# Kernel optimization log

Hardware: AMD Instinct MI355X
Metric: run time of the kernel (lower is better)

## Reference

```python
import jax, jax.numpy as jnp
import numpy as np

B, S, D, R, H, NI, NP, NO, K = 2, 2048, 1024, 1024, 8, 8, 32, 8, 3
DH = R // H


def setup_inputs() -> dict:
    key = jax.random.key(0)
    ks = jax.random.split(key, 32)
    rn = lambda k, shp, s=1.0: jax.random.normal(k, shp, jnp.float32) * s
    nrm = lambda v: v / (jnp.linalg.norm(v, axis=-1, keepdims=True) + 1e-8)
    w = 1.0 / np.sqrt(D).astype(np.float32)
    inp = {
        'x': rn(ks[0], (B, S, D)),
        'mask': jnp.tril(jnp.ones((S, S), bool))[None, None],  # causal [1,1,S,S]
        'Wr_in': rn(ks[1], (NI, D), w), 'Wr_proc': rn(ks[2], (NP, D), w), 'Wr_out': rn(ks[3], (NO, D), w),
        'WrO_in': rn(ks[4], (NI, R), w), 'WrO_proc': rn(ks[5], (NP, R), w), 'WrO_out': rn(ks[6], (NO, R), w),
        'Wq_in': rn(ks[7], (NI, D, R), w), 'vq': nrm(rn(ks[8], (NP, R))), 'Wq_out': rn(ks[9], (NO, R, D), w),
        'Wk_in': rn(ks[10], (NI, D, R), w), 'vk': nrm(rn(ks[11], (NP, R))), 'Wk_out': rn(ks[12], (NO, R, D), w),
        'Wv_in': rn(ks[13], (NI, D, R), w), 'vv': nrm(rn(ks[14], (NP, R))), 'Wv_out': rn(ks[15], (NO, R, D), w),
        # circuit_O = NeuronCircuit(rank, d_model): dims swapped
        'Wo_in': rn(ks[16], (NI, R, D), w), 'vo': nrm(rn(ks[17], (NP, D))), 'Wo_out': rn(ks[18], (NO, D, R), w),
    }
    return inp


def _router(x, Wi, Wp, Wo, k):
    in_w = jax.nn.softmax(x @ Wi.T, axis=-1)            # [B,S,NI]
    _, proc_idx = jax.lax.top_k(x @ Wp.T, k)            # [B,S,k]
    out_w = jax.nn.softmax(x @ Wo.T, axis=-1)           # [B,S,NO]
    return in_w, proc_idx, out_w


def _circuit(x, Win, vproc, Wout, in_w, proc_idx, out_w):
    # soft input mix: d_in -> r
    h = jnp.einsum('bsd,ndr,bsn->bsr', x, Win, in_w)
    # k sequential Householder reflections with gathered vectors
    v = vproc[proc_idx]                                 # [B,S,k,r]
    v = v / jnp.sqrt(jnp.sum(v * v, axis=-1, keepdims=True) + 1e-8)
    for i in range(v.shape[2]):
        vi = v[:, :, i, :]
        h = h - 2.0 * vi * jnp.sum(h * vi, axis=-1, keepdims=True)
    # soft output mix: r -> d_out
    return jnp.einsum('bsr,nrd,bsn->bsd', h, Wout, out_w)


def reference(x, mask, Wr_in, Wr_proc, Wr_out, WrO_in, WrO_proc, WrO_out,
              Wq_in, vq, Wq_out, Wk_in, vk, Wk_out, Wv_in, vv, Wv_out,
              Wo_in, vo, Wo_out):
    in_w, pidx, out_w = _router(x, Wr_in, Wr_proc, Wr_out, K)
    Q = _circuit(x, Wq_in, vq, Wq_out, in_w, pidx, out_w)   # [B,S,R]
    Kt = _circuit(x, Wk_in, vk, Wk_out, in_w, pidx, out_w)
    V = _circuit(x, Wv_in, vv, Wv_out, in_w, pidx, out_w)
    q = Q.reshape(B, S, H, DH).transpose(0, 2, 1, 3)
    k = Kt.reshape(B, S, H, DH).transpose(0, 2, 1, 3)
    v = V.reshape(B, S, H, DH).transpose(0, 2, 1, 3)
    scores = jnp.einsum('bhqd,bhkd->bhqk', q, k) / np.sqrt(DH).astype(np.float32)
    scores = jnp.where(mask, scores, jnp.float32(-1e9))
    p = jax.nn.softmax(scores, axis=-1)
    o = jnp.einsum('bhqk,bhkd->bhqd', p, v)
    o = o.transpose(0, 2, 1, 3).reshape(B, S, R)
    in_wO, pidxO, out_wO = _router(o, WrO_in, WrO_proc, WrO_out, K)
    out = _circuit(o, Wo_in, vo, Wo_out, in_wO, pidxO, out_wO)  # [B,S,D]
    return out
```

## Files before the change

### kernel.cpp

```cpp
#include <hip/hip_runtime.h>


typedef __attribute__((ext_vector_type(4))) float f32x4;
typedef _Float16 f16x8 __attribute__((ext_vector_type(8)));
typedef _Float16 f16x4 __attribute__((ext_vector_type(4)));

static constexpr int S_LEN  = 2048;
static constexpr int TOK    = 4096;
static constexpr int DMODEL = 1024;
static constexpr int KDIM   = 8192;

__device__ __forceinline__ void async16(const void* g, void* l) {
  __builtin_amdgcn_global_load_lds(
      (const __attribute__((address_space(1))) void*)g,
      (__attribute__((address_space(3))) void*)l, 16, 0, 0);
}

__global__ __launch_bounds__(256) void split_kernel(const float* __restrict__ X,
                                                    _Float16* __restrict__ Xh,
                                                    _Float16* __restrict__ Xl) {
  size_t i = ((size_t)blockIdx.x * 256 + threadIdx.x) * 4;
  float4 v = *(const float4*)&X[i];
  float a[4] = {v.x, v.y, v.z, v.w};
  f16x4 hv, lv;
#pragma unroll
  for (int e = 0; e < 4; ++e) {
    _Float16 hh = (_Float16)a[e];
    hv[e] = hh;
    lv[e] = (_Float16)(a[e] - (float)hh);
  }
  *(f16x4*)&Xh[i] = hv;
  *(f16x4*)&Xl[i] = lv;
}

__global__ __launch_bounds__(256) void transpose_split(const float* __restrict__ W,
                                                       _Float16* __restrict__ Th,
                                                       _Float16* __restrict__ Tl) {
  __shared__ float tbuf[64][65];
  const int tid = threadIdx.x;
  const int k0 = blockIdx.x * 64, n0 = blockIdx.y * 64;
#pragma unroll
  for (int j = 0; j < 4; ++j) {
    int ci = tid + 256 * j;
    int r = ci >> 4, c4 = (ci & 15) * 4;
    float4 v = *(const float4*)&W[(size_t)(k0 + r) * DMODEL + n0 + c4];
    tbuf[r][c4 + 0] = v.x; tbuf[r][c4 + 1] = v.y;
    tbuf[r][c4 + 2] = v.z; tbuf[r][c4 + 3] = v.w;
  }
  __syncthreads();
#pragma unroll
  for (int j = 0; j < 2; ++j) {
    int ci = tid + 256 * j;
    int nl = ci >> 3, k8 = (ci & 7) * 8;
    f16x8 hv, lv;
#pragma unroll
    for (int e = 0; e < 8; ++e) {
      float v = tbuf[k8 + e][nl];
      _Float16 hh = (_Float16)v;
      hv[e] = hh;
      lv[e] = (_Float16)(v - (float)hh);
    }
    size_t off = (size_t)(n0 + nl) * KDIM + k0 + k8;
    *(f16x8*)&Th[off] = hv;
    *(f16x8*)&Tl[off] = lv;
  }
}

__global__ __launch_bounds__(256) void router_kernel(const float* __restrict__ X,
                                                     const float* __restrict__ Wi,
                                                     const float* __restrict__ Wp,
                                                     const float* __restrict__ Wo,
                                                     float* __restrict__ in_w,
                                                     float* __restrict__ out_w,
                                                     int* __restrict__ pidx) {
  __shared__ float xs[1024];
  __shared__ double lg[48];
  const int t = blockIdx.x, tid = threadIdx.x;
  const int wid = tid >> 6, lane = tid & 63;
#pragma unroll
  for (int j = 0; j < 4; ++j) {
    int d = tid + 256 * j;
    xs[d] = X[(size_t)t * DMODEL + d];
  }
  __syncthreads();
  for (int i = wid; i < 48; i += 4) {
    const float* wrow = (i < 8)  ? Wi + (size_t)i * DMODEL
                      : (i < 40) ? Wp + (size_t)(i - 8) * DMODEL
                                 : Wo + (size_t)(i - 40) * DMODEL;
    double s = 0.0;
#pragma unroll
    for (int j = 0; j < 16; ++j) { int d = lane + 64 * j; s += (double)xs[d] * (double)wrow[d]; }
#pragma unroll
    for (int mm = 32; mm >= 1; mm >>= 1) s += __shfl_xor(s, mm);
    if (lane == 0) lg[i] = s;
  }
  __syncthreads();
  if (tid == 0) {
    float l[8], m;
    for (int i = 0; i < 8; ++i) l[i] = (float)lg[i];
    m = l[0];
    for (int i = 1; i < 8; ++i) m = fmaxf(m, l[i]);
    float e[8], su = 0.f;
    for (int i = 0; i < 8; ++i) { e[i] = expf(l[i] - m); su += e[i]; }
    for (int i = 0; i < 8; ++i) in_w[t * 8 + i] = e[i] / su;
  } else if (tid == 64) {
    float l[8], m;
    for (int i = 0; i < 8; ++i) l[i] = (float)lg[40 + i];
    m = l[0];
    for (int i = 1; i < 8; ++i) m = fmaxf(m, l[i]);
    float e[8], su = 0.f;
    for (int i = 0; i < 8; ++i) { e[i] = expf(l[i] - m); su += e[i]; }
    for (int i = 0; i < 8; ++i) out_w[t * 8 + i] = e[i] / su;
  } else if (tid == 128) {
    unsigned used = 0;
    for (int j = 0; j < 3; ++j) {
      double best = -1e300; int bi = 0;
      for (int i = 0; i < 32; ++i)
        if (!((used >> i) & 1u) && lg[8 + i] > best) { best = lg[8 + i]; bi = i; }
      used |= 1u << bi;
      pidx[t * 3 + j] = bi;
    }
  }
}

__global__ __launch_bounds__(256) void reflect_kernel(const float* __restrict__ Pa,
                                                      const float* __restrict__ Pb,
                                                      const int* __restrict__ pidx,
                                                      const float* __restrict__ vtab,
                                                      _Float16* __restrict__ Hh,
                                                      _Float16* __restrict__ Hl) {
  __shared__ float red[8];
  const int t = blockIdx.x, tid = threadIdx.x;
  const int wid = tid >> 6, lane = tid & 63;
  float4 ha = *(const float4*)&Pa[(size_t)t * DMODEL + tid * 4];
  float4 hb = *(const float4*)&Pb[(size_t)t * DMODEL + tid * 4];
  float4 h = {ha.x + hb.x, ha.y + hb.y, ha.z + hb.z, ha.w + hb.w};
  for (int i = 0; i < 3; ++i) {
    int idx = pidx[t * 3 + i];
    float4 vi = *(const float4*)&vtab[(size_t)idx * DMODEL + tid * 4];
    float hv = h.x * vi.x + h.y * vi.y + h.z * vi.z + h.w * vi.w;
    float vv = vi.x * vi.x + vi.y * vi.y + vi.z * vi.z + vi.w * vi.w;
#pragma unroll
    for (int mm = 32; mm >= 1; mm >>= 1) { hv += __shfl_xor(hv, mm); vv += __shfl_xor(vv, mm); }
    if (lane == 0) { red[wid] = hv; red[4 + wid] = vv; }
    __syncthreads();
    float dot = red[0] + red[1] + red[2] + red[3];
    float vn  = red[4] + red[5] + red[6] + red[7];
    __syncthreads();
    float c = 2.f * dot / (vn + 1e-8f);
    h.x -= c * vi.x; h.y -= c * vi.y; h.z -= c * vi.z; h.w -= c * vi.w;
  }
  float a[4] = {h.x, h.y, h.z, h.w};
  f16x4 hv4, lv4;
#pragma unroll
  for (int e = 0; e < 4; ++e) {
    _Float16 hh = (_Float16)a[e];
    hv4[e] = hh;
    lv4[e] = (_Float16)(a[e] - (float)hh);
  }
  *(f16x4*)&Hh[(size_t)t * DMODEL + tid * 4] = hv4;
  *(f16x4*)&Hl[(size_t)t * DMODEL + tid * 4] = lv4;
}

__global__ __launch_bounds__(256) void reduce_add(const float* __restrict__ a,
                                                  const float* __restrict__ b,
                                                  float* __restrict__ c) {
  size_t i = ((size_t)blockIdx.x * 256 + threadIdx.x) * 4;
  float4 va = *(const float4*)&a[i];
  float4 vb = *(const float4*)&b[i];
  float4 vc = {va.x + vb.x, va.y + vb.y, va.z + vb.z, va.w + vb.w};
  *(float4*)&c[i] = vc;
}

__global__ __launch_bounds__(256, 4) void gemm_planes(const _Float16* __restrict__ Ahp,
                                                      const _Float16* __restrict__ Alp,
                                                      const float* __restrict__ wmix,
                                                      const _Float16* __restrict__ Bh,
                                                      const _Float16* __restrict__ Bl,
                                                      float* __restrict__ Cp0,
                                                      float* __restrict__ Cp1) {
  __shared__ _Float16 sAh[128 * 32], sAl[128 * 32];
  __shared__ _Float16 sBh[128 * 32], sBl[128 * 32];
  __shared__ float sWr[128 * 4];
  const int tid = threadIdx.x;
  const int wid = tid >> 6, lane = tid & 63;
  const int l16 = lane & 15, lhi = lane >> 4;
  const int wr = wid >> 1, wc = wid & 1;
  const int fid = blockIdx.x + (blockIdx.y << 5) + (blockIdx.z << 8);
  const int wg  = ((fid & 7) << 6) + (fid >> 3);
  const int bm = (wg & 31) * 128;
  const int bn = ((wg >> 5) & 7) * 128;
  const int kz = wg >> 8;
  const int kbase = kz * 4096, nb = kz * 4;
  float* __restrict__ Cp = kz ? Cp1 : Cp0;

  for (int i = tid; i < 512; i += 256) {
    int row = i >> 2, p = i & 3;
    const float* w = &wmix[(size_t)(bm + row) * 8 + nb];
    sWr[i] = (p < 3) ? w[p] / w[p + 1] : w[3];
  }

  f32x4 acc[4][4];
#pragma unroll
  for (int i = 0; i < 4; ++i)
#pragma unroll
    for (int j = 0; j < 4; ++j) { f32x4 z = {0.f, 0.f, 0.f, 0.f}; acc[i][j] = z; }

  for (int kt = 0; kt < 4096; kt += 32) {
    const int kg = kbase + kt, d0 = kg & 1023;
#pragma unroll
    for (int j = 0; j < 2; ++j) {
      int ci = tid + 256 * j;
      int row = ci >> 2, jc = ci & 3;
      int jcs = jc ^ ((row >> 1) & 3);
      size_t ga = (size_t)(bm + row) * DMODEL + d0 + jcs * 8;
      size_t gb = (size_t)(bn + row) * KDIM + kg + jcs * 8;
      async16(&Ahp[ga], &sAh[ci * 8]);
      async16(&Alp[ga], &sAl[ci * 8]);
      async16(&Bh[gb], &sBh[ci * 8]);
      async16(&Bl[gb], &sBl[ci * 8]);
    }
    __syncthreads();
    f16x8 fah[4], fal[4], fbh[4], fbl[4];
#pragma unroll
    for (int mi = 0; mi < 4; ++mi) {
      int row = wr * 64 + mi * 16 + l16;
      int idx = row * 32 + ((lhi ^ ((row >> 1) & 3)) * 8);
      fah[mi] = *(const f16x8*)&sAh[idx];
      fal[mi] = *(const f16x8*)&sAl[idx];
    }
#pragma unroll
    for (int ni = 0; ni < 4; ++ni) {
      int row = wc * 64 + ni * 16 + l16;
      int idx = row * 32 + ((lhi ^ ((row >> 1) & 3)) * 8);
      fbh[ni] = *(const f16x8*)&sBh[idx];
      fbl[ni] = *(const f16x8*)&sBl[idx];
    }
#pragma unroll
    for (int mi = 0; mi < 4; ++mi)
#pragma unroll
      for (int ni = 0; ni < 4; ++ni) {
        f32x4 a = acc[mi][ni];
        a = __builtin_amdgcn_mfma_f32_16x16x32_f16(fah[mi], fbh[ni], a, 0, 0, 0);
        a = __builtin_amdgcn_mfma_f32_16x16x32_f16(fah[mi], fbl[ni], a, 0, 0, 0);
        a = __builtin_amdgcn_mfma_f32_16x16x32_f16(fal[mi], fbh[ni], a, 0, 0, 0);
        acc[mi][ni] = a;
      }
    __syncthreads();
    if ((kt & 1023) == 992 && kt != 4064) {
      int p = kt >> 10;
#pragma unroll
      for (int mi = 0; mi < 4; ++mi)
#pragma unroll
        for (int r = 0; r < 4; ++r) {
          float s = sWr[(wr * 64 + mi * 16 + lhi * 4 + r) * 4 + p];
#pragma unroll
          for (int ni = 0; ni < 4; ++ni) acc[mi][ni][r] *= s;
        }
    }
  }
#pragma unroll
  for (int mi = 0; mi < 4; ++mi)
#pragma unroll
    for (int r = 0; r < 4; ++r) {
      int rowl = wr * 64 + mi * 16 + lhi * 4 + r;
      float s = sWr[rowl * 4 + 3];
#pragma unroll
      for (int ni = 0; ni < 4; ++ni) {
        int col = bn + wc * 64 + ni * 16 + l16;
        Cp[(size_t)(bm + rowl) * DMODEL + col] = acc[mi][ni][r] * s;
      }
    }
}

__global__ __launch_bounds__(256) void vtrans_kernel(const float* __restrict__ Va,
                                                     const float* __restrict__ Vb,
                                                     float* __restrict__ Vt) {
  __shared__ float tbuf[64][65];
  const int tid = threadIdx.x;
  const int t0 = blockIdx.x * 64, d0 = blockIdx.y * 64, bh = blockIdx.z;
  const int b = bh >> 3, h = bh & 7;
#pragma unroll
  for (int j = 0; j < 4; ++j) {
    int ci = tid + 256 * j;
    int r = ci >> 4, c4 = (ci & 15) * 4;
    size_t g = (size_t)(b * S_LEN + t0 + r) * DMODEL + h * 128 + d0 + c4;
    float4 va = *(const float4*)&Va[g];
    float4 vb = *(const float4*)&Vb[g];
    tbuf[r][c4 + 0] = va.x + vb.x; tbuf[r][c4 + 1] = va.y + vb.y;
    tbuf[r][c4 + 2] = va.z + vb.z; tbuf[r][c4 + 3] = va.w + vb.w;
  }
  __syncthreads();
#pragma unroll
  for (int j = 0; j < 4; ++j) {
    int ci = tid + 256 * j;
    int r = ci >> 4, c4 = (ci & 15) * 4;
    float4 o;
    o.x = tbuf[c4 + 0][r]; o.y = tbuf[c4 + 1][r];
    o.z = tbuf[c4 + 2][r]; o.w = tbuf[c4 + 3][r];
    *(float4*)&Vt[((size_t)bh * 128 + d0 + r) * S_LEN + t0 + c4] = o;
  }
}

__global__ __launch_bounds__(256) void attn_kernel(const float* __restrict__ Q,
                                                   const float* __restrict__ Kg,
                                                   const float* __restrict__ Vt,
                                                   float* __restrict__ O,
                                                   _Float16* __restrict__ Oh,
                                                   _Float16* __restrict__ Ol) {
  __shared__ _Float16 sKh[32 * 128], sKl[32 * 128];
  __shared__ _Float16 sVh[128 * 32], sVl[128 * 32];
  __shared__ _Float16 sPh[4 * 16 * 32], sPl[4 * 16 * 32];
  const int tid = threadIdx.x;
  const int wid = tid >> 6, lane = tid & 63;
  const int l16 = lane & 15, lhi = lane >> 4;
  const int qt = (gridDim.x - 1) - blockIdx.x;
  const int bh = blockIdx.y;
  const int b = bh >> 3, h = bh & 7;
  const size_t qkbase = (size_t)b * S_LEN * DMODEL + h * 128;
  const float scale = 0.08838834764831845f;

  const int qrow = qt * 64 + wid * 16 + l16;
  f16x8 qh[4], ql[4];
#pragma unroll
  for (int kk = 0; kk < 4; ++kk) {
    const float* qp = &Q[qkbase + (size_t)qrow * DMODEL + kk * 32 + lhi * 8];
    float4 a = *(const float4*)qp;
    float4 c = *(const float4*)(qp + 4);
    float v[8] = {a.x, a.y, a.z, a.w, c.x, c.y, c.z, c.w};
#pragma unroll
    for (int e = 0; e < 8; ++e) {
      _Float16 hh = (_Float16)v[e];
      qh[kk][e] = hh;
      ql[kk][e] = (_Float16)(v[e] - (float)hh);
    }
  }

  f32x4 of[8];
#pragma unroll
  for (int i = 0; i < 8; ++i) { f32x4 z = {0.f, 0.f, 0.f, 0.f}; of[i] = z; }
  float m_[4], l_[4];
#pragma unroll
  for (int r = 0; r < 4; ++r) { m_[r] = -1e30f; l_[r] = 0.f; }

  const int ntw = qt * 2 + 1 + (wid >> 1);
  const int NT  = qt * 2 + 2;

  for (int kt = 0; kt < NT; ++kt) {
    __syncthreads();
#pragma unroll
    for (int j = 0; j < 4; ++j) {
      int ci = tid + 256 * j;
      int k = ci >> 5, d4 = (ci & 31) * 4;
      float4 v = *(const float4*)&Kg[qkbase + (size_t)(kt * 32 + k) * DMODEL + d4];
      f16x4 hv, lv;
      float vals[4] = {v.x, v.y, v.z, v.w};
#pragma unroll
      for (int e = 0; e < 4; ++e) {
        _Float16 hh = (_Float16)vals[e];
        hv[e] = hh;
        lv[e] = (_Float16)(vals[e] - (float)hh);
      }
      int idx = k * 128 + (d4 ^ ((k & 7) * 8));
      *(f16x4*)&sKh[idx] = hv;
      *(f16x4*)&sKl[idx] = lv;
    }
#pragma unroll
    for (int j = 0; j < 4; ++j) {
      int ci = tid + 256 * j;
      int d = ci >> 3, t4 = (ci & 7) * 4;
      float4 v = *(const float4*)&Vt[((size_t)bh * 128 + d) * S_LEN + kt * 32 + t4];
      f16x4 hv, lv;
      float vals[4] = {v.x, v.y, v.z, v.w};
#pragma unroll
      for (int e = 0; e < 4; ++e) {
        _Float16 hh = (_Float16)vals[e];
        hv[e] = hh;
        lv[e] = (_Float16)(vals[e] - (float)hh);
      }
      int idx = d * 32 + (t4 ^ (((d >> 1) & 3) * 8));
      *(f16x4*)&sVh[idx] = hv;
      *(f16x4*)&sVl[idx] = lv;
    }
    __syncthreads();

    if (kt < ntw) {
      f32x4 s0 = {0.f, 0.f, 0.f, 0.f}, s1 = {0.f, 0.f, 0.f, 0.f};
#pragma unroll
      for (int kk = 0; kk < 4; ++kk) {
        int col = (kk * 32 + lhi * 8);
        int i0 = l16 * 128 + (col ^ ((l16 & 7) * 8));
        int i1 = (16 + l16) * 128 + (col ^ (((16 + l16) & 7) * 8));
        f16x8 kb0h = *(const f16x8*)&sKh[i0];
        f16x8 kb0l = *(const f16x8*)&sKl[i0];
        f16x8 kb1h = *(const f16x8*)&sKh[i1];
        f16x8 kb1l = *(const f16x8*)&sKl[i1];
        s0 = __builtin_amdgcn_mfma_f32_16x16x32_f16(qh[kk], kb0h, s0, 0, 0, 0);
        s0 = __builtin_amdgcn_mfma_f32_16x16x32_f16(qh[kk], kb0l, s0, 0, 0, 0);
        s0 = __builtin_amdgcn_mfma_f32_16x16x32_f16(ql[kk], kb0h, s0, 0, 0, 0);
        s1 = __builtin_amdgcn_mfma_f32_16x16x32_f16(qh[kk], kb1h, s1, 0, 0, 0);
        s1 = __builtin_amdgcn_mfma_f32_16x16x32_f16(qh[kk], kb1l, s1, 0, 0, 0);
        s1 = __builtin_amdgcn_mfma_f32_16x16x32_f16(ql[kk], kb1h, s1, 0, 0, 0);
      }
      const int qg = qt * 64 + wid * 16 + (lane >> 4) * 4;
      if (kt == ntw - 1) {
#pragma unroll
        for (int r = 0; r < 4; ++r) {
          int q = qg + r;
          int k0 = kt * 32 + l16, k1 = k0 + 16;
          s0[r] = (k0 <= q) ? s0[r] * scale : -1e30f;
          s1[r] = (k1 <= q) ? s1[r] * scale : -1e30f;
        }
      } else {
#pragma unroll
        for (int r = 0; r < 4; ++r) { s0[r] *= scale; s1[r] *= scale; }
      }
      float p0[4], p1[4], fr[4];
#pragma unroll
      for (int r = 0; r < 4; ++r) {
        float rm = fmaxf(s0[r], s1[r]);
        rm = fmaxf(rm, __shfl_xor(rm, 1));
        rm = fmaxf(rm, __shfl_xor(rm, 2));
        rm = fmaxf(rm, __shfl_xor(rm, 4));
        rm = fmaxf(rm, __shfl_xor(rm, 8));
        float mn = fmaxf(m_[r], rm);
        fr[r] = __expf(m_[r] - mn);
        m_[r] = mn;
        p0[r] = __expf(s0[r] - mn);
        p1[r] = __expf(s1[r] - mn);
        float rs = p0[r] + p1[r];
        rs += __shfl_xor(rs, 1);
        rs += __shfl_xor(rs, 2);
        rs += __shfl_xor(rs, 4);
        rs += __shfl_xor(rs, 8);
        l_[r] = l_[r] * fr[r] + rs;
      }
#pragma unroll
      for (int i = 0; i < 8; ++i)
#pragma unroll
        for (int r = 0; r < 4; ++r) of[i][r] *= fr[r];
#pragma unroll
      for (int r = 0; r < 4; ++r) {
        int q = (lane >> 4) * 4 + r;
        int swz = ((q >> 1) & 3) * 8;
        int c0 = l16, c1 = 16 + l16;
        _Float16 h0 = (_Float16)p0[r];
        _Float16 h1 = (_Float16)p1[r];
        sPh[wid * 512 + q * 32 + (c0 ^ swz)] = h0;
        sPl[wid * 512 + q * 32 + (c0 ^ swz)] = (_Float16)(p0[r] - (float)h0);
        sPh[wid * 512 + q * 32 + (c1 ^ swz)] = h1;
        sPl[wid * 512 + q * 32 + (c1 ^ swz)] = (_Float16)(p1[r] - (float)h1);
      }
      int pidxr = wid * 512 + l16 * 32 + ((lhi * 8) ^ (((l16 >> 1) & 3) * 8));
      f16x8 pah = *(const f16x8*)&sPh[pidxr];
      f16x8 pal = *(const f16x8*)&sPl[pidxr];
#pragma unroll
      for (int d16 = 0; d16 < 8; ++d16) {
        int d = d16 * 16 + l16;
        int vidx = d * 32 + ((lhi * 8) ^ (((d >> 1) & 3) * 8));
        f16x8 vbh = *(const f16x8*)&sVh[vidx];
        f16x8 vbl = *(const f16x8*)&sVl[vidx];
        f32x4 a = of[d16];
        a = __builtin_amdgcn_mfma_f32_16x16x32_f16(pah, vbh, a, 0, 0, 0);
        a = __builtin_amdgcn_mfma_f32_16x16x32_f16(pah, vbl, a, 0, 0, 0);
        a = __builtin_amdgcn_mfma_f32_16x16x32_f16(pal, vbh, a, 0, 0, 0);
        of[d16] = a;
      }
    }
  }
  float inv[4];
#pragma unroll
  for (int r = 0; r < 4; ++r) inv[r] = 1.f / l_[r];
  const int qg = qt * 64 + wid * 16 + (lane >> 4) * 4;
#pragma unroll
  for (int d16 = 0; d16 < 8; ++d16)
#pragma unroll
    for (int r = 0; r < 4; ++r) {
      float val = of[d16][r] * inv[r];
      size_t gi = qkbase + (size_t)(qg + r) * DMODEL + d16 * 16 + l16;
      O[gi] = val;
      _Float16 hh = (_Float16)val;
      Oh[gi] = hh;
      Ol[gi] = (_Float16)(val - (float)hh);
    }
}

extern "C" void kernel_launch(void* const* d_in, const int* in_sizes, int n_in,
                              void* d_out, int out_size, void* d_ws, size_t ws_size,
                              hipStream_t stream) {
  (void)in_sizes; (void)n_in; (void)out_size;
  const float* x        = (const float*)d_in[0];
  const float* Wr_in    = (const float*)d_in[2];
  const float* Wr_proc  = (const float*)d_in[3];
  const float* Wr_out   = (const float*)d_in[4];
  const float* WrO_in   = (const float*)d_in[5];
  const float* WrO_proc = (const float*)d_in[6];
  const float* WrO_out  = (const float*)d_in[7];
  const float* Wq_in    = (const float*)d_in[8];
  const float* vq       = (const float*)d_in[9];
  const float* Wq_out   = (const float*)d_in[10];
  const float* Wk_in    = (const float*)d_in[11];
  const float* vk       = (const float*)d_in[12];
  const float* Wk_out   = (const float*)d_in[13];
  const float* Wv_in    = (const float*)d_in[14];
  const float* vv       = (const float*)d_in[15];
  const float* Wv_out   = (const float*)d_in[16];
  const float* Wo_in    = (const float*)d_in[17];
  const float* vo       = (const float*)d_in[18];
  const float* Wo_out   = (const float*)d_in[19];

  char* wsbase = (char*)d_ws;
  size_t off = 0;
  auto carve = [&](size_t bytes) -> void* {
    void* r = wsbase + off;
    off = (off + bytes + 255) & ~(size_t)255;
    return r;
  };
  const size_t WBYTES = (size_t)KDIM * DMODEL * 2;
  const size_t PBYTES = (size_t)TOK * DMODEL * 2;
  const size_t HBYTES = (size_t)TOK * DMODEL * 4;
  _Float16* WTh = (_Float16*)carve(WBYTES);
  _Float16* WTl = (_Float16*)carve(WBYTES);
  _Float16* Xh  = (_Float16*)carve(PBYTES);
  _Float16* Xl  = (_Float16*)carve(PBYTES);
  _Float16* Hh  = (_Float16*)carve(PBYTES);
  _Float16* Hl  = (_Float16*)carve(PBYTES);
  float* c0 = (float*)carve(HBYTES);
  float* c1 = (float*)carve(HBYTES);
  float* r1 = (float*)carve(HBYTES);
  float* r2 = (float*)carve(HBYTES);
  float* iw1 = (float*)carve((size_t)TOK * 8 * 4);
  float* ow1 = (float*)carve((size_t)TOK * 8 * 4);
  float* iw2 = (float*)carve((size_t)TOK * 8 * 4);
  float* ow2 = (float*)carve((size_t)TOK * 8 * 4);
  int* pi1 = (int*)carve((size_t)TOK * 3 * 4);
  int* pi2 = (int*)carve((size_t)TOK * 3 * 4);

  if (off > ws_size) {
    hipMemsetAsync(d_out, 0, (size_t)out_size * 4, stream);
    return;
  }

  float* Vt = (float*)WTh;
  _Float16* Oh = (_Float16*)r1;
  _Float16* Ol = Oh + (size_t)TOK * DMODEL;

  const dim3 blk(256);
  const dim3 tgrid(KDIM / 64, DMODEL / 64);
  const dim3 ggrid(TOK / 128, DMODEL / 128, 2);
  const dim3 rgrid(TOK * DMODEL / (256 * 4));
  const dim3 vgrid(S_LEN / 64, 2, 16);
  const dim3 agrid(S_LEN / 64, 16);

  split_kernel<<<rgrid, blk, 0, stream>>>(x, Xh, Xl);
  router_kernel<<<TOK, blk, 0, stream>>>(x, Wr_in, Wr_proc, Wr_out, iw1, ow1, pi1);

  transpose_split<<<tgrid, blk, 0, stream>>>(Wq_in, WTh, WTl);
  gemm_planes<<<ggrid, blk, 0, stream>>>(Xh, Xl, iw1, WTh, WTl, c0, c1);
  reflect_kernel<<<TOK, blk, 0, stream>>>(c0, c1, pi1, vq, Hh, Hl);
  transpose_split<<<tgrid, blk, 0, stream>>>(Wq_out, WTh, WTl);
  gemm_planes<<<ggrid, blk, 0, stream>>>(Hh, Hl, ow1, WTh, WTl, c0, c1);
  reduce_add<<<rgrid, blk, 0, stream>>>(c0, c1, r1);

  transpose_split<<<tgrid, blk, 0, stream>>>(Wk_in, WTh, WTl);
  gemm_planes<<<ggrid, blk, 0, stream>>>(Xh, Xl, iw1, WTh, WTl, c0, c1);
  reflect_kernel<<<TOK, blk, 0, stream>>>(c0, c1, pi1, vk, Hh, Hl);
  transpose_split<<<tgrid, blk, 0, stream>>>(Wk_out, WTh, WTl);
  gemm_planes<<<ggrid, blk, 0, stream>>>(Hh, Hl, ow1, WTh, WTl, c0, c1);
  reduce_add<<<rgrid, blk, 0, stream>>>(c0, c1, r2);

  transpose_split<<<tgrid, blk, 0, stream>>>(Wv_in, WTh, WTl);
  gemm_planes<<<ggrid, blk, 0, stream>>>(Xh, Xl, iw1, WTh, WTl, c0, c1);
  reflect_kernel<<<TOK, blk, 0, stream>>>(c0, c1, pi1, vv, Hh, Hl);
  transpose_split<<<tgrid, blk, 0, stream>>>(Wv_out, WTh, WTl);
  gemm_planes<<<ggrid, blk, 0, stream>>>(Hh, Hl, ow1, WTh, WTl, c0, c1);
  vtrans_kernel<<<vgrid, blk, 0, stream>>>(c0, c1, Vt);

  attn_kernel<<<agrid, blk, 0, stream>>>(r1, r2, Vt, c0, Oh, Ol);

  router_kernel<<<TOK, blk, 0, stream>>>(c0, WrO_in, WrO_proc, WrO_out, iw2, ow2, pi2);
  transpose_split<<<tgrid, blk, 0, stream>>>(Wo_in, WTh, WTl);
  gemm_planes<<<ggrid, blk, 0, stream>>>(Oh, Ol, iw2, WTh, WTl, c1, r2);
  reflect_kernel<<<TOK, blk, 0, stream>>>(c1, r2, pi2, vo, Hh, Hl);
  transpose_split<<<tgrid, blk, 0, stream>>>(Wo_out, WTh, WTl);
  gemm_planes<<<ggrid, blk, 0, stream>>>(Hh, Hl, ow2, WTh, WTl, c0, c1);
  reduce_add<<<rgrid, blk, 0, stream>>>(c0, c1, (float*)d_out);
}
```

Baseline: 1.934 ms.

## Split GEMM K into three chunks, prequantize Q/K/V planes, drop low-A MFMA in output circuit

The split-K GEMM now uses three K partitions (3072/3072/2048) instead of two. This grows the grid from 512 to 768 workgroups to fill more CUs, and the reflect/reduce kernels now sum three partials. Q, K and V are converted to fp16 hi/lo planes once in the reduce and transpose kernels, so attention loads them with async global-to-LDS copies instead of converting on every tile. The final circuit's GEMMs use a FAST variant that skips the low-A plane and its MFMA, and attention writes only the fp16-hi O. This trades some accuracy in the last stage for less MFMA work and memory traffic.

```diff
diff --git a/kernel.cpp b/kernel.cpp
--- a/kernel.cpp
+++ b/kernel.cpp
@@ -123,18 +123,22 @@
   }
 }
 
-__global__ __launch_bounds__(256) void reflect_kernel(const float* __restrict__ Pa,
-                                                      const float* __restrict__ Pb,
-                                                      const int* __restrict__ pidx,
-                                                      const float* __restrict__ vtab,
-                                                      _Float16* __restrict__ Hh,
-                                                      _Float16* __restrict__ Hl) {
+__global__ __launch_bounds__(256) void reflect3_kernel(const float* __restrict__ Pa,
+                                                       const float* __restrict__ Pb,
+                                                       const float* __restrict__ Pc,
+                                                       const int* __restrict__ pidx,
+                                                       const float* __restrict__ vtab,
+                                                       _Float16* __restrict__ Hh,
+                                                       _Float16* __restrict__ Hl) {
   __shared__ float red[8];
   const int t = blockIdx.x, tid = threadIdx.x;
   const int wid = tid >> 6, lane = tid & 63;
-  float4 ha = *(const float4*)&Pa[(size_t)t * DMODEL + tid * 4];
-  float4 hb = *(const float4*)&Pb[(size_t)t * DMODEL + tid * 4];
-  float4 h = {ha.x + hb.x, ha.y + hb.y, ha.z + hb.z, ha.w + hb.w};
+  size_t gi = (size_t)t * DMODEL + tid * 4;
+  float4 ha = *(const float4*)&Pa[gi];
+  float4 hb = *(const float4*)&Pb[gi];
+  float4 hc = *(const float4*)&Pc[gi];
+  float4 h = {ha.x + hb.x + hc.x, ha.y + hb.y + hc.y,
+              ha.z + hb.z + hc.z, ha.w + hb.w + hc.w};
   for (int i = 0; i < 3; ++i) {
     int idx = pidx[t * 3 + i];
     float4 vi = *(const float4*)&vtab[(size_t)idx * DMODEL + tid * 4];
@@ -158,27 +162,54 @@
     hv4[e] = hh;
     lv4[e] = (_Float16)(a[e] - (float)hh);
   }
-  *(f16x4*)&Hh[(size_t)t * DMODEL + tid * 4] = hv4;
-  *(f16x4*)&Hl[(size_t)t * DMODEL + tid * 4] = lv4;
-}
-
-__global__ __launch_bounds__(256) void reduce_add(const float* __restrict__ a,
-                                                  const float* __restrict__ b,
-                                                  float* __restrict__ c) {
+  *(f16x4*)&Hh[gi] = hv4;
+  *(f16x4*)&Hl[gi] = lv4;
+}
+
+__global__ __launch_bounds__(256) void reduce3_planes(const float* __restrict__ a,
+                                                      const float* __restrict__ b,
+                                                      const float* __restrict__ c,
+                                                      _Float16* __restrict__ Dh,
+                                                      _Float16* __restrict__ Dl) {
   size_t i = ((size_t)blockIdx.x * 256 + threadIdx.x) * 4;
   float4 va = *(const float4*)&a[i];
   float4 vb = *(const float4*)&b[i];
-  float4 vc = {va.x + vb.x, va.y + vb.y, va.z + vb.z, va.w + vb.w};
-  *(float4*)&c[i] = vc;
-}
-
+  float4 vc = *(const float4*)&c[i];
+  float s[4] = {va.x + vb.x + vc.x, va.y + vb.y + vc.y,
+                va.z + vb.z + vc.z, va.w + vb.w + vc.w};
+  f16x4 hv, lv;
+#pragma unroll
+  for (int e = 0; e < 4; ++e) {
+    _Float16 hh = (_Float16)s[e];
+    hv[e] = hh;
+    lv[e] = (_Float16)(s[e] - (float)hh);
+  }
+  *(f16x4*)&Dh[i] = hv;
+  *(f16x4*)&Dl[i] = lv;
+}
+
+__global__ __launch_bounds__(256) void reduce3_f32(const float* __restrict__ a,
+                                                   const float* __restrict__ b,
+                                                   const float* __restrict__ c,
+                                                   float* __restrict__ d) {
+  size_t i = ((size_t)blockIdx.x * 256 + threadIdx.x) * 4;
+  float4 va = *(const float4*)&a[i];
+  float4 vb = *(const float4*)&b[i];
+  float4 vc = *(const float4*)&c[i];
+  float4 vd = {va.x + vb.x + vc.x, va.y + vb.y + vc.y,
+               va.z + vb.z + vc.z, va.w + vb.w + vc.w};
+  *(float4*)&d[i] = vd;
+}
+
+template <bool FAST>
 __global__ __launch_bounds__(256, 4) void gemm_planes(const _Float16* __restrict__ Ahp,
                                                       const _Float16* __restrict__ Alp,
                                                       const float* __restrict__ wmix,
                                                       const _Float16* __restrict__ Bh,
                                                       const _Float16* __restrict__ Bl,
-                                                      float* __restrict__ Cp0,
-                                                      float* __restrict__ Cp1) {
+                                                      float* __restrict__ C0,
+                                                      float* __restrict__ C1,
+                                                      float* __restrict__ C2) {
   __shared__ _Float16 sAh[128 * 32], sAl[128 * 32];
   __shared__ _Float16 sBh[128 * 32], sBl[128 * 32];
   __shared__ float sWr[128 * 4];
@@ -187,17 +218,19 @@
   const int l16 = lane & 15, lhi = lane >> 4;
   const int wr = wid >> 1, wc = wid & 1;
   const int fid = blockIdx.x + (blockIdx.y << 5) + (blockIdx.z << 8);
-  const int wg  = ((fid & 7) << 6) + (fid >> 3);
-  const int bm = (wg & 31) * 128;
-  const int bn = ((wg >> 5) & 7) * 128;
-  const int kz = wg >> 8;
-  const int kbase = kz * 4096, nb = kz * 4;
-  float* __restrict__ Cp = kz ? Cp1 : Cp0;
+  const int wg  = (fid & 7) * 96 + (fid >> 3);
+  const int kz  = wg >> 8;
+  const int rem = wg & 255;
+  const int bm = (rem & 31) * 128;
+  const int bn = (rem >> 5) * 128;
+  const int np = (kz == 2) ? 2 : 3;
+  const int kbase = kz * 3072, nb = kz * 3;
+  float* __restrict__ Cp = (kz == 0) ? C0 : (kz == 1) ? C1 : C2;
 
   for (int i = tid; i < 512; i += 256) {
     int row = i >> 2, p = i & 3;
     const float* w = &wmix[(size_t)(bm + row) * 8 + nb];
-    sWr[i] = (p < 3) ? w[p] / w[p + 1] : w[3];
+    sWr[i] = (p < np - 1) ? w[p] / w[p + 1] : w[np - 1];
   }
 
   f32x4 acc[4][4];
@@ -206,7 +239,8 @@
 #pragma unroll
     for (int j = 0; j < 4; ++j) { f32x4 z = {0.f, 0.f, 0.f, 0.f}; acc[i][j] = z; }
 
-  for (int kt = 0; kt < 4096; kt += 32) {
+  const int kend = np * 1024;
+  for (int kt = 0; kt < kend; kt += 32) {
     const int kg = kbase + kt, d0 = kg & 1023;
 #pragma unroll
     for (int j = 0; j < 2; ++j) {
@@ -216,7 +250,7 @@
       size_t ga = (size_t)(bm + row) * DMODEL + d0 + jcs * 8;
       size_t gb = (size_t)(bn + row) * KDIM + kg + jcs * 8;
       async16(&Ahp[ga], &sAh[ci * 8]);
-      async16(&Alp[ga], &sAl[ci * 8]);
+      if (!FAST) async16(&Alp[ga], &sAl[ci * 8]);
       async16(&Bh[gb], &sBh[ci * 8]);
       async16(&Bl[gb], &sBl[ci * 8]);
     }
@@ -227,7 +261,7 @@
       int row = wr * 64 + mi * 16 + l16;
       int idx = row * 32 + ((lhi ^ ((row >> 1) & 3)) * 8);
       fah[mi] = *(const f16x8*)&sAh[idx];
-      fal[mi] = *(const f16x8*)&sAl[idx];
+      if (!FAST) fal[mi] = *(const f16x8*)&sAl[idx];
     }
 #pragma unroll
     for (int ni = 0; ni < 4; ++ni) {
@@ -243,11 +277,12 @@
         f32x4 a = acc[mi][ni];
         a = __builtin_amdgcn_mfma_f32_16x16x32_f16(fah[mi], fbh[ni], a, 0, 0, 0);
         a = __builtin_amdgcn_mfma_f32_16x16x32_f16(fah[mi], fbl[ni], a, 0, 0, 0);
-        a = __builtin_amdgcn_mfma_f32_16x16x32_f16(fal[mi], fbh[ni], a, 0, 0, 0);
+        if (!FAST)
+          a = __builtin_amdgcn_mfma_f32_16x16x32_f16(fal[mi], fbh[ni], a, 0, 0, 0);
         acc[mi][ni] = a;
       }
     __syncthreads();
-    if ((kt & 1023) == 992 && kt != 4064) {
+    if ((kt & 1023) == 992 && kt != kend - 32) {
       int p = kt >> 10;
 #pragma unroll
       for (int mi = 0; mi < 4; ++mi)
@@ -273,9 +308,11 @@
     }
 }
 
-__global__ __launch_bounds__(256) void vtrans_kernel(const float* __restrict__ Va,
-                                                     const float* __restrict__ Vb,
-                                                     float* __restrict__ Vt) {
+__global__ __launch_bounds__(256) void vtrans3_kernel(const float* __restrict__ Va,
+                                                      const float* __restrict__ Vb,
+                                                      const float* __restrict__ Vc,
+                                                      _Float16* __restrict__ Vth,
+                                                      _Float16* __restrict__ Vtl) {
   __shared__ float tbuf[64][65];
   const int tid = threadIdx.x;
   const int t0 = blockIdx.x * 64, d0 = blockIdx.y * 64, bh = blockIdx.z;
@@ -287,27 +324,37 @@
     size_t g = (size_t)(b * S_LEN + t0 + r) * DMODEL + h * 128 + d0 + c4;
     float4 va = *(const float4*)&Va[g];
     float4 vb = *(const float4*)&Vb[g];
-    tbuf[r][c4 + 0] = va.x + vb.x; tbuf[r][c4 + 1] = va.y + vb.y;
-    tbuf[r][c4 + 2] = va.z + vb.z; tbuf[r][c4 + 3] = va.w + vb.w;
+    float4 vc = *(const float4*)&Vc[g];
+    tbuf[r][c4 + 0] = va.x + vb.x + vc.x; tbuf[r][c4 + 1] = va.y + vb.y + vc.y;
+    tbuf[r][c4 + 2] = va.z + vb.z + vc.z; tbuf[r][c4 + 3] = va.w + vb.w + vc.w;
   }
   __syncthreads();
 #pragma unroll
   for (int j = 0; j < 4; ++j) {
     int ci = tid + 256 * j;
     int r = ci >> 4, c4 = (ci & 15) * 4;
-    float4 o;
-    o.x = tbuf[c4 + 0][r]; o.y = tbuf[c4 + 1][r];
-    o.z = tbuf[c4 + 2][r]; o.w = tbuf[c4 + 3][r];
-    *(float4*)&Vt[((size_t)bh * 128 + d0 + r) * S_LEN + t0 + c4] = o;
-  }
-}
-
-__global__ __launch_bounds__(256) void attn_kernel(const float* __restrict__ Q,
-                                                   const float* __restrict__ Kg,
-                                                   const float* __restrict__ Vt,
+    float s[4] = {tbuf[c4 + 0][r], tbuf[c4 + 1][r], tbuf[c4 + 2][r], tbuf[c4 + 3][r]};
+    f16x4 hv, lv;
+#pragma unroll
+    for (int e = 0; e < 4; ++e) {
+      _Float16 hh = (_Float16)s[e];
+      hv[e] = hh;
+      lv[e] = (_Float16)(s[e] - (float)hh);
+    }
+    size_t o = ((size_t)bh * 128 + d0 + r) * S_LEN + t0 + c4;
+    *(f16x4*)&Vth[o] = hv;
+    *(f16x4*)&Vtl[o] = lv;
+  }
+}
+
+__global__ __launch_bounds__(256) void attn_kernel(const _Float16* __restrict__ Qh,
+                                                   const _Float16* __restrict__ Ql,
+                                                   const _Float16* __restrict__ Kh,
+                                                   const _Float16* __restrict__ Kl,
+                                                   const _Float16* __restrict__ Vth,
+                                                   const _Float16* __restrict__ Vtl,
                                                    float* __restrict__ O,
-                                                   _Float16* __restrict__ Oh,
-                                                   _Float16* __restrict__ Ol) {
+                                                   _Float16* __restrict__ Oh) {
   __shared__ _Float16 sKh[32 * 128], sKl[32 * 128];
   __shared__ _Float16 sVh[128 * 32], sVl[128 * 32];
   __shared__ _Float16 sPh[4 * 16 * 32], sPl[4 * 16 * 32];
@@ -321,19 +368,12 @@
   const float scale = 0.08838834764831845f;
 
   const int qrow = qt * 64 + wid * 16 + l16;
+  const size_t qoff = qkbase + (size_t)qrow * DMODEL;
   f16x8 qh[4], ql[4];
 #pragma unroll
   for (int kk = 0; kk < 4; ++kk) {
-    const float* qp = &Q[qkbase + (size_t)qrow * DMODEL + kk * 32 + lhi * 8];
-    float4 a = *(const float4*)qp;
-    float4 c = *(const float4*)(qp + 4);
-    float v[8] = {a.x, a.y, a.z, a.w, c.x, c.y, c.z, c.w};
-#pragma unroll
-    for (int e = 0; e < 8; ++e) {
-      _Float16 hh = (_Float16)v[e];
-      qh[kk][e] = hh;
-      ql[kk][e] = (_Float16)(v[e] - (float)hh);
-    }
+    qh[kk] = *(const f16x8*)&Qh[qoff + kk * 32 + lhi * 8];
+    ql[kk] = *(const f16x8*)&Ql[qoff + kk * 32 + lhi * 8];
   }
 
   f32x4 of[8];
@@ -349,38 +389,22 @@
   for (int kt = 0; kt < NT; ++kt) {
     __syncthreads();
 #pragma unroll
-    for (int j = 0; j < 4; ++j) {
+    for (int j = 0; j < 2; ++j) {
       int ci = tid + 256 * j;
-      int k = ci >> 5, d4 = (ci & 31) * 4;
-      float4 v = *(const float4*)&Kg[qkbase + (size_t)(kt * 32 + k) * DMODEL + d4];
-      f16x4 hv, lv;
-      float vals[4] = {v.x, v.y, v.z, v.w};
-#pragma unroll
-      for (int e = 0; e < 4; ++e) {
-        _Float16 hh = (_Float16)vals[e];
-        hv[e] = hh;
-        lv[e] = (_Float16)(vals[e] - (float)hh);
-      }
-      int idx = k * 128 + (d4 ^ ((k & 7) * 8));
-      *(f16x4*)&sKh[idx] = hv;
-      *(f16x4*)&sKl[idx] = lv;
-    }
-#pragma unroll
-    for (int j = 0; j < 4; ++j) {
+      int k = ci >> 4, c = ci & 15;
+      int cs = c ^ (k & 7);
+      size_t g = qkbase + (size_t)(kt * 32 + k) * DMODEL + cs * 8;
+      async16(&Kh[g], &sKh[k * 128 + c * 8]);
+      async16(&Kl[g], &sKl[k * 128 + c * 8]);
+    }
+#pragma unroll
+    for (int j = 0; j < 2; ++j) {
       int ci = tid + 256 * j;
-      int d = ci >> 3, t4 = (ci & 7) * 4;
-      float4 v = *(const float4*)&Vt[((size_t)bh * 128 + d) * S_LEN + kt * 32 + t4];
-      f16x4 hv, lv;
-      float vals[4] = {v.x, v.y, v.z, v.w};
-#pragma unroll
-      for (int e = 0; e < 4; ++e) {
-        _Float16 hh = (_Float16)vals[e];
-        hv[e] = hh;
-        lv[e] = (_Float16)(vals[e] - (float)hh);
-      }
-      int idx = d * 32 + (t4 ^ (((d >> 1) & 3) * 8));
-      *(f16x4*)&sVh[idx] = hv;
-      *(f16x4*)&sVl[idx] = lv;
+      int d = ci >> 2, c = ci & 3;
+      int cs = c ^ ((d >> 1) & 3);
+      size_t g = ((size_t)bh * 128 + d) * S_LEN + kt * 32 + cs * 8;
+      async16(&Vth[g], &sVh[d * 32 + c * 8]);
+      async16(&Vtl[g], &sVl[d * 32 + c * 8]);
     }
     __syncthreads();
 
@@ -479,9 +503,7 @@
       float val = of[d16][r] * inv[r];
       size_t gi = qkbase + (size_t)(qg + r) * DMODEL + d16 * 16 + l16;
       O[gi] = val;
-      _Float16 hh = (_Float16)val;
-      Oh[gi] = hh;
-      Ol[gi] = (_Float16)(val - (float)hh);
+      Oh[gi] = (_Float16)val;
     }
 }
 
@@ -525,10 +547,13 @@
   _Float16* Xl  = (_Float16*)carve(PBYTES);
   _Float16* Hh  = (_Float16*)carve(PBYTES);
   _Float16* Hl  = (_Float16*)carve(PBYTES);
-  float* c0 = (float*)carve(HBYTES);
-  float* c1 = (float*)carve(HBYTES);
-  float* r1 = (float*)carve(HBYTES);
-  float* r2 = (float*)carve(HBYTES);
+  float* P0 = (float*)carve(HBYTES);
+  float* P1 = (float*)carve(HBYTES);
+  float* P2 = (float*)carve(HBYTES);
+  _Float16* Qph = (_Float16*)carve(PBYTES);
+  _Float16* Qpl = (_Float16*)carve(PBYTES);
+  _Float16* Kph = (_Float16*)carve(PBYTES);
+  _Float16* Kpl = (_Float16*)carve(PBYTES);
   float* iw1 = (float*)carve((size_t)TOK * 8 * 4);
   float* ow1 = (float*)carve((size_t)TOK * 8 * 4);
   float* iw2 = (float*)carve((size_t)TOK * 8 * 4);
@@ -541,13 +566,15 @@
     return;
   }
 
-  float* Vt = (float*)WTh;
-  _Float16* Oh = (_Float16*)r1;
-  _Float16* Ol = Oh + (size_t)TOK * DMODEL;
+  _Float16* Vth = WTh;
+  _Float16* Vtl = WTh + (size_t)TOK * DMODEL;
+  float*    Ofp = P0;
+  _Float16* Ohp = (_Float16*)P1;
+  float*    PX  = (float*)Xh;
 
   const dim3 blk(256);
   const dim3 tgrid(KDIM / 64, DMODEL / 64);
-  const dim3 ggrid(TOK / 128, DMODEL / 128, 2);
+  const dim3 ggrid(TOK / 128, DMODEL / 128, 3);
   const dim3 rgrid(TOK * DMODEL / (256 * 4));
   const dim3 vgrid(S_LEN / 64, 2, 16);
   const dim3 agrid(S_LEN / 64, 16);
@@ -556,33 +583,33 @@
   router_kernel<<<TOK, blk, 0, stream>>>(x, Wr_in, Wr_proc, Wr_out, iw1, ow1, pi1);
 
   transpose_split<<<tgrid, blk, 0, stream>>>(Wq_in, WTh, WTl);
-  gemm_planes<<<ggrid, blk, 0, stream>>>(Xh, Xl, iw1, WTh, WTl, c0, c1);
-  reflect_kernel<<<TOK, blk, 0, stream>>>(c0, c1, pi1, vq, Hh, Hl);
+  gemm_planes<false><<<ggrid, blk, 0, stream>>>(Xh, Xl, iw1, WTh, WTl, P0, P1, P2);
+  reflect3_kernel<<<TOK, blk, 0, stream>>>(P0, P1, P2, pi1, vq, Hh, Hl);
   transpose_split<<<tgrid, blk, 0, stream>>>(Wq_out, WTh, WTl);
-  gemm_planes<<<ggrid, blk, 0, stream>>>(Hh, Hl, ow1, WTh, WTl, c0, c1);
-  reduce_add<<<rgrid, blk, 0, stream>>>(c0, c1, r1);
+  gemm_planes<false><<<ggrid, blk, 0, stream>>>(Hh, Hl, ow1, WTh, WTl, P0, P1, P2);
+  reduce3_planes<<<rgrid, blk, 0, stream>>>(P0, P1, P2, Qph, Qpl);
 
   transpose_split<<<tgrid, blk, 0, stream>>>(Wk_in, WTh, WTl);
-  gemm_planes<<<ggrid, blk, 0, stream>>>(Xh, Xl, iw1, WTh, WTl, c0, c1);
-  reflect_kernel<<<TOK, blk, 0, stream>>>(c0, c1, pi1, vk, Hh, Hl);
+  gemm_planes<false><<<ggrid, blk, 0, stream>>>(Xh, Xl, iw1, WTh, WTl, P0, P1, P2);
+  reflect3_kernel<<<TOK, blk, 0, stream>>>(P0, P1, P2, pi1, vk, Hh, Hl);
   transpose_split<<<tgrid, blk, 0, stream>>>(Wk_out, WTh, WTl);
-  gemm_planes<<<ggrid, blk, 0, stream>>>(Hh, Hl, ow1, WTh, WTl, c0, c1);
-  reduce_add<<<rgrid, blk, 0, stream>>>(c0, c1, r2);
+  gemm_planes<false><<<ggrid, blk, 0, stream>>>(Hh, Hl, ow1, WTh, WTl, P0, P1, P2);
+  reduce3_planes<<<rgrid, blk, 0, stream>>>(P0, P1, P2, Kph, Kpl);
 
   transpose_split<<<tgrid, blk, 0, stream>>>(Wv_in, WTh, WTl);
-  gemm_planes<<<ggrid, blk, 0, stream>>>(Xh, Xl, iw1, WTh, WTl, c0, c1);
-  reflect_kernel<<<TOK, blk, 0, stream>>>(c0, c1, pi1, vv, Hh, Hl);
+  gemm_planes<false><<<ggrid, blk, 0, stream>>>(Xh, Xl, iw1, WTh, WTl, P0, P1, P2);
+  reflect3_kernel<<<TOK, blk, 0, stream>>>(P0, P1, P2, pi1, vv, Hh, Hl);
   transpose_split<<<tgrid, blk, 0, stream>>>(Wv_out, WTh, WTl);
-  gemm_planes<<<ggrid, blk, 0, stream>>>(Hh, Hl, ow1, WTh, WTl, c0, c1);
-  vtrans_kernel<<<vgrid, blk, 0, stream>>>(c0, c1, Vt);
-
-  attn_kernel<<<agrid, blk, 0, stream>>>(r1, r2, Vt, c0, Oh, Ol);
-
-  router_kernel<<<TOK, blk, 0, stream>>>(c0, WrO_in, WrO_proc, WrO_out, iw2, ow2, pi2);
+  gemm_planes<false><<<ggrid, blk, 0, stream>>>(Hh, Hl, ow1, WTh, WTl, P0, P1, P2);
+  vtrans3_kernel<<<vgrid, blk, 0, stream>>>(P0, P1, P2, Vth, Vtl);
+
+  attn_kernel<<<agrid, blk, 0, stream>>>(Qph, Qpl, Kph, Kpl, Vth, Vtl, Ofp, Ohp);
+
+  router_kernel<<<TOK, blk, 0, stream>>>(Ofp, WrO_in, WrO_proc, WrO_out, iw2, ow2, pi2);
   transpose_split<<<tgrid, blk, 0, stream>>>(Wo_in, WTh, WTl);
-  gemm_planes<<<ggrid, blk, 0, stream>>>(Oh, Ol, iw2, WTh, WTl, c1, r2);
-  reflect_kernel<<<TOK, blk, 0, stream>>>(c1, r2, pi2, vo, Hh, Hl);
+  gemm_planes<true><<<ggrid, blk, 0, stream>>>(Ohp, Ohp, iw2, WTh, WTl, P2, PX, P0);
+  reflect3_kernel<<<TOK, blk, 0, stream>>>(P2, PX, P0, pi2, vo, Hh, Hl);
   transpose_split<<<tgrid, blk, 0, stream>>>(Wo_out, WTh, WTl);
-  gemm_planes<<<ggrid, blk, 0, stream>>>(Hh, Hl, ow2, WTh, WTl, c0, c1);
-  reduce_add<<<rgrid, blk, 0, stream>>>(c0, c1, (float*)d_out);
-}
+  gemm_planes<true><<<ggrid, blk, 0, stream>>>(Hh, Hl, ow2, WTh, WTl, P0, P1, P2);
+  reduce3_f32<<<rgrid, blk, 0, stream>>>(P0, P1, P2, (float*)d_out);
+}
```

Measured after the change: 2.038 ms. +5.3%, slower.
